# Kernel tuning notes

Hardware: AMD Instinct MI355X
Metric: run time of the kernel (lower is better)

The kernel has to match this reference:

```python
import jax, jax.numpy as jnp
import numpy as np

NUM_HEADS = 12


def get_rel_pos(q_size, k_size, rel_pos):
    # rel_pos: (2*max(q,k)-1, head_dim); sizes match table here so no resize.
    max_rel_dist = int(2 * max(q_size, k_size) - 1)
    if rel_pos.shape[0] != max_rel_dist:
        rel_pos = jax.image.resize(rel_pos, (max_rel_dist, rel_pos.shape[1]), method='linear')
    q_coords = jnp.arange(q_size)[:, None] * max(k_size / q_size, 1.0)
    k_coords = jnp.arange(k_size)[None, :] * max(q_size / k_size, 1.0)
    rel = (q_coords - k_coords + (k_size - 1) * max(q_size / k_size, 1.0)).astype(jnp.int32)
    return rel_pos[rel.reshape(-1)].reshape(q_size, k_size, -1)  # (q, k, head_dim)


def setup_inputs() -> dict:
    key = jax.random.key(0)
    ks = jax.random.split(key, 7)
    B, H, W, C = 8, 32, 32, 768
    head_dim = C // NUM_HEADS
    return {
        'x': jax.random.normal(ks[0], (B, H, W, C), jnp.float32),
        'w_qkv': jax.random.normal(ks[1], (C, 3 * C), jnp.float32) * 0.02,
        'b_qkv': jnp.zeros((3 * C,), jnp.float32),
        'rel_pos_h': jax.random.normal(ks[2], (2 * H - 1, head_dim), jnp.float32) * 0.02,
        'rel_pos_w': jax.random.normal(ks[3], (2 * W - 1, head_dim), jnp.float32) * 0.02,
        'w_proj': jax.random.normal(ks[4], (C, C), jnp.float32) * 0.02,
        'b_proj': jnp.zeros((C,), jnp.float32),
    }


def reference(x, w_qkv, b_qkv, rel_pos_h, rel_pos_w, w_proj, b_proj):
    B, H, W, C = x.shape
    heads = NUM_HEADS
    hd = C // heads
    S = H * W
    qkv = x @ w_qkv + b_qkv                                  # (B,H,W,3C)
    qkv = qkv.reshape(B, S, 3, heads, hd).transpose(2, 0, 3, 1, 4)
    qkv = qkv.reshape(3, B * heads, S, hd)
    q, k, v = qkv[0], qkv[1], qkv[2]
    attn = (q * hd ** -0.5) @ k.transpose(0, 2, 1)           # (B*heads, S, S)
    rh = get_rel_pos(H, H, rel_pos_h)                        # (H,H,hd)
    rw = get_rel_pos(W, W, rel_pos_w)                        # (W,W,hd)
    r_q = q.reshape(B * heads, H, W, hd)
    rel_h = jnp.einsum('bhwc,hkc->bhwk', r_q, rh)
    rel_w = jnp.einsum('bhwc,wkc->bhwk', r_q, rw)
    attn = (attn.reshape(B * heads, H, W, H, W)
            + rel_h[:, :, :, :, None]
            + rel_w[:, :, :, None, :]).reshape(B * heads, S, S)
    attn = jax.nn.softmax(attn, axis=-1)
    out = (attn @ v).reshape(B, heads, H, W, hd).transpose(0, 2, 3, 1, 4).reshape(B, H, W, C)
    return out @ w_proj + b_proj
```

## Files before the change

kernel.cpp:

```cpp
#include <hip/hip_runtime.h>
#include <hip/hip_bf16.h>

#define BATCH 8
#define SEQ   1024
#define CH    768
#define NH    12
#define HD    64
#define BH    96
#define N_QKV 2304

#define LOG2E 1.44269504088896f

typedef __attribute__((ext_vector_type(8))) short bfrag;
typedef __attribute__((ext_vector_type(4))) short short4v;
typedef __attribute__((ext_vector_type(4))) float ffrag;
typedef __attribute__((ext_vector_type(4))) int  intv4;

__device__ __forceinline__ short f2bf(float x) {
    __hip_bfloat16 h = __float2bfloat16(x);
    return *reinterpret_cast<short*>(&h);
}
__device__ __forceinline__ float bf2f(short b) {
    __hip_bfloat16 h;
    *reinterpret_cast<short*>(&h) = b;
    return __bfloat162float(h);
}
__device__ __forceinline__ void split2(float x, short& hi, short& lo) {
    short h = f2bf(x);
    hi = h;
    lo = f2bf(x - bf2f(h));
}
__device__ __forceinline__ void async_copy16(void* lds, const void* g) {
    __builtin_amdgcn_global_load_lds(
        (const __attribute__((address_space(1))) void*)g,
        (__attribute__((address_space(3))) void*)lds, 16, 0, 0);
}
__device__ __forceinline__ void pinned_load16(intv4& dst, const void* p) {
    asm volatile("global_load_dwordx4 %0, %1, off"
                 : "=&v"(dst) : "v"((unsigned long long)p));
}

__global__ __launch_bounds__(256) void prep(
    const float* __restrict__ x,
    const float* __restrict__ w_qkv, const float* __restrict__ w_proj,
    short* __restrict__ Xh,
    short* __restrict__ WqhT,
    short* __restrict__ WphT, short* __restrict__ WplT)
{
    __shared__ float ts[32][33];
    const int tid = threadIdx.x;
    const int bid = blockIdx.x;

    if (bid < 512) {
        const int n4 = (BATCH * SEQ * CH) / 4;
        for (int i = bid * 256 + tid; i < n4; i += 512 * 256) {
            float4 f = ((const float4*)x)[i];
            short4v h;
            h[0] = f2bf(f.x); h[1] = f2bf(f.y); h[2] = f2bf(f.z); h[3] = f2bf(f.w);
            ((short4v*)Xh)[i] = h;
        }
        return;
    }
    if (bid < 2240) {
        int t = bid - 512;
        const int bx = t % 72, by = t / 72;
        const int r0 = by * 32, c0 = bx * 32;
        #pragma unroll
        for (int i = 0; i < 4; ++i) {
            int idx = tid + i * 256;
            int rr = idx >> 5, cc = idx & 31;
            ts[rr][cc] = w_qkv[(size_t)(r0 + rr) * N_QKV + c0 + cc];
        }
        __syncthreads();
        #pragma unroll
        for (int i = 0; i < 4; ++i) {
            int idx = tid + i * 256;
            int rr = idx >> 5, cc = idx & 31;
            WqhT[(size_t)(c0 + rr) * CH + r0 + cc] = f2bf(ts[cc][rr]);
        }
        return;
    }
    {
        int t = bid - 2240;
        const int bx = t % 24, by = t / 24;
        const int r0 = by * 32, c0 = bx * 32;
        #pragma unroll
        for (int i = 0; i < 4; ++i) {
            int idx = tid + i * 256;
            int rr = idx >> 5, cc = idx & 31;
            ts[rr][cc] = w_proj[(size_t)(r0 + rr) * CH + c0 + cc];
        }
        __syncthreads();
        #pragma unroll
        for (int i = 0; i < 4; ++i) {
            int idx = tid + i * 256;
            int rr = idx >> 5, cc = idx & 31;
            short h, l;
            split2(ts[cc][rr], h, l);
            WphT[(size_t)(c0 + rr) * CH + r0 + cc] = h;
            WplT[(size_t)(c0 + rr) * CH + r0 + cc] = l;
        }
    }
}

__device__ __forceinline__ void gemm_core1(
    short* lds,
    const short* __restrict__ Ah, const short* __restrict__ BhT,
    int m0, int n0, ffrag acc[4][4])
{
    const int tid = threadIdx.x;
    const int wave = tid >> 6, lane = tid & 63;
    const int quad = lane >> 4, l16 = lane & 15;
    const int wm = (wave & 1) * 64, wn = (wave >> 1) * 64;

    const int arr  = wave >> 1;
    const int half = wave & 1;
    const short* src = arr ? BhT : Ah;
    const int row0 = (arr ? n0 : m0) + half * 64;
    const size_t lane_off = (size_t)(lane >> 3) * CH + (size_t)((lane & 7) ^ (lane >> 3)) * 8;
    const short* sbase = src + (size_t)row0 * CH + lane_off;
    short* ldsw = lds + arr * 8192 + half * 4096;

    for (int c = 0; c < 12; ++c) {
        __syncthreads();
        #pragma unroll
        for (int i = 0; i < 8; ++i)
            async_copy16(ldsw + i * 512, sbase + (size_t)i * 8 * CH + c * 64);
        __syncthreads();

        #pragma unroll
        for (int kc = 0; kc < 2; ++kc) {
            bfrag ah[4], bh[4];
            const int xs = ((kc * 4 + quad) ^ (l16 & 7)) * 8;
            #pragma unroll
            for (int i = 0; i < 4; ++i) {
                ah[i] = *(const bfrag*)&lds[(wm + i * 16 + l16) * 64 + xs];
                bh[i] = *(const bfrag*)&lds[8192 + (wn + i * 16 + l16) * 64 + xs];
            }
            #pragma unroll
            for (int mi = 0; mi < 4; ++mi)
                #pragma unroll
                for (int ni = 0; ni < 4; ++ni)
                    acc[mi][ni] = __builtin_amdgcn_mfma_f32_16x16x32_bf16(ah[mi], bh[ni], acc[mi][ni], 0, 0, 0);
        }
    }
}

__device__ __forceinline__ void gemm_core3(
    short* lds,
    const short* __restrict__ Ah, const short* __restrict__ Al,
    const short* __restrict__ BhT, const short* __restrict__ BlT,
    int m0, int n0, ffrag acc[4][4])
{
    const int tid = threadIdx.x;
    const int wave = tid >> 6, lane = tid & 63;
    const int quad = lane >> 4, l16 = lane & 15;
    const int wm = (wave & 1) * 64, wn = (wave >> 1) * 64;

    const short* src;
    int row0;
    if (wave == 0)      { src = Ah;  row0 = m0; }
    else if (wave == 1) { src = Al;  row0 = m0; }
    else if (wave == 2) { src = BhT; row0 = n0; }
    else                { src = BlT; row0 = n0; }
    const size_t lane_off = (size_t)(lane >> 3) * CH + (size_t)((lane & 7) ^ (lane >> 3)) * 8;
    const short* sbase = src + (size_t)row0 * CH + lane_off;
    short* ldsw = lds + wave * 8192;

    for (int c = 0; c < 12; ++c) {
        __syncthreads();
        #pragma unroll
        for (int i = 0; i < 16; ++i)
            async_copy16(ldsw + i * 512, sbase + (size_t)i * 8 * CH + c * 64);
        __syncthreads();

        #pragma unroll
        for (int kc = 0; kc < 2; ++kc) {
            bfrag ah[4], al[4], bh[4], bl[4];
            const int xs = ((kc * 4 + quad) ^ (l16 & 7)) * 8;
            #pragma unroll
            for (int i = 0; i < 4; ++i) {
                int ra = (wm + i * 16 + l16) * 64 + xs;
                int rb = (wn + i * 16 + l16) * 64 + xs;
                ah[i] = *(const bfrag*)&lds[ra];
                al[i] = *(const bfrag*)&lds[8192 + ra];
                bh[i] = *(const bfrag*)&lds[16384 + rb];
                bl[i] = *(const bfrag*)&lds[24576 + rb];
            }
            #pragma unroll
            for (int mi = 0; mi < 4; ++mi)
                #pragma unroll
                for (int ni = 0; ni < 4; ++ni) {
                    acc[mi][ni] = __builtin_amdgcn_mfma_f32_16x16x32_bf16(ah[mi], bh[ni], acc[mi][ni], 0, 0, 0);
                    acc[mi][ni] = __builtin_amdgcn_mfma_f32_16x16x32_bf16(ah[mi], bl[ni], acc[mi][ni], 0, 0, 0);
                    acc[mi][ni] = __builtin_amdgcn_mfma_f32_16x16x32_bf16(al[mi], bh[ni], acc[mi][ni], 0, 0, 0);
                }
        }
    }
}

__global__ __launch_bounds__(256) void gemm_qkv_mfma(
    const short* __restrict__ Xh,
    const short* __restrict__ WhT,
    const float* __restrict__ bias,
    short* __restrict__ qh, short* __restrict__ kh, short* __restrict__ vT)
{
    __shared__ short lds[2 * 8192];
    const int id  = blockIdx.x;
    const int xcd = id & 7;
    const int per = id >> 3;
    const int mi_ = per / 9, ni_ = per % 9;
    const int m0 = ((xcd & 3) * 16 + mi_) * 128;
    const int n0 = ((xcd >> 2) * 9 + ni_) * 128;
    const int which = n0 / CH;

    ffrag acc[4][4];
    #pragma unroll
    for (int i = 0; i < 4; ++i)
        #pragma unroll
        for (int j = 0; j < 4; ++j) acc[i][j] = (ffrag){0.f, 0.f, 0.f, 0.f};

    gemm_core1(lds, Xh, WhT, m0, n0, acc);

    const int tid = threadIdx.x;
    const int wave = tid >> 6, lane = tid & 63;
    const int quad = lane >> 4, l16 = lane & 15;
    const int wm = (wave & 1) * 64, wn = (wave >> 1) * 64;
    const int b = m0 >> 10;

    #pragma unroll
    for (int ni = 0; ni < 4; ++ni) {
        int n = n0 + wn + ni * 16 + l16;
        float bv = bias[n];
        int nin = n - which * CH;
        int head = nin >> 6, d = nin & 63;
        #pragma unroll
        for (int mi = 0; mi < 4; ++mi) {
            if (which == 2) {
                int s_base = (m0 & 1023) + wm + mi * 16 + quad * 4;
                short4v pk;
                #pragma unroll
                for (int r = 0; r < 4; ++r) pk[r] = f2bf(acc[mi][ni][r] + bv);
                *(short4v*)&vT[((size_t)(b * NH + head) * HD + d) * SEQ + s_base] = pk;
            } else {
                const float scale = (which == 0) ? 0.125f * LOG2E : 1.0f;
                short* dst = (which == 0) ? qh : kh;
                #pragma unroll
                for (int r = 0; r < 4; ++r) {
                    int m = m0 + wm + mi * 16 + quad * 4 + r;
                    int s = m & 1023;
                    dst[((size_t)(b * NH + head) * SEQ + s) * HD + d] =
                        f2bf((acc[mi][ni][r] + bv) * scale);
                }
            }
        }
    }
}

__global__ __launch_bounds__(256) void gemm_proj_mfma(
    const short* __restrict__ Ah, const short* __restrict__ Al,
    const short* __restrict__ WhT, const short* __restrict__ WlT,
    const float* __restrict__ bias, float* __restrict__ out)
{
    __shared__ short lds[4 * 8192];
    const int id  = blockIdx.x;
    const int xcd = id & 7;
    const int per = id >> 3;
    const int m0 = (xcd * 8 + per / 6) * 128;
    const int n0 = (per % 6) * 128;

    ffrag acc[4][4];
    #pragma unroll
    for (int i = 0; i < 4; ++i)
        #pragma unroll
        for (int j = 0; j < 4; ++j) acc[i][j] = (ffrag){0.f, 0.f, 0.f, 0.f};

    gemm_core3(lds, Ah, Al, WhT, WlT, m0, n0, acc);

    const int tid = threadIdx.x;
    const int wave = tid >> 6, lane = tid & 63;
    const int quad = lane >> 4, l16 = lane & 15;
    const int wm = (wave & 1) * 64, wn = (wave >> 1) * 64;

    #pragma unroll
    for (int ni = 0; ni < 4; ++ni) {
        int n = n0 + wn + ni * 16 + l16;
        float bv = bias[n];
        #pragma unroll
        for (int mi = 0; mi < 4; ++mi)
            #pragma unroll
            for (int r = 0; r < 4; ++r) {
                int m = m0 + wm + mi * 16 + quad * 4 + r;
                out[(size_t)m * CH + n] = acc[mi][ni][r] + bv;
            }
    }
}

__global__ __launch_bounds__(256, 3) void attn_kernel(
    const short* __restrict__ qh,
    const short* __restrict__ kh_g, const short* __restrict__ vT_g,
    const float* __restrict__ rph,
    const float* __restrict__ rpw,
    short* __restrict__ aoh, short* __restrict__ aol)
{
    const int fid   = blockIdx.x;
    const int xcd   = fid & 7;
    const int inner = fid >> 3;
    const int s0    = (inner & 7) * 128;
    const int bh    = xcd * 12 + (inner >> 3);

    const int tid  = threadIdx.x;
    const int wave = tid >> 6;
    const int lane = tid & 63;
    const int quad = lane >> 4;
    const int l16  = lane & 15;

    __shared__ short Kh[64 * 64];
    __shared__ short Vth[64 * 64];
    __shared__ short Th[128][68];
    __shared__ short Tw_Ps[128 * 68];

    const size_t bh_koff = (size_t)bh * SEQ * HD;
    const size_t bh_voff = (size_t)bh * HD * SEQ;
    const size_t klane = (size_t)(lane >> 3) * HD + (size_t)((lane & 7) ^ (lane >> 3)) * 8;
    const size_t vlane = (size_t)(lane >> 3) * SEQ + (size_t)((lane & 7) ^ (lane >> 3)) * 8;

    const short* kbase = kh_g + bh_koff + klane;
    const short* vbase = vT_g + bh_voff + vlane;
    const int i0 = wave * 2;
    short* KhW0 = Kh  + i0 * 512 + lane * 8;
    short* VtW0 = Vth + i0 * 512 + lane * 8;

    intv4 kA0, kA1, vA0, vA1, kB0, kB1, vB0, vB1;
    pinned_load16(kA0, kbase + (size_t)(i0 * 8) * HD);
    pinned_load16(kA1, kbase + (size_t)(i0 * 8 + 8) * HD);
    pinned_load16(vA0, vbase + (size_t)(i0 * 8) * SEQ);
    pinned_load16(vA1, vbase + (size_t)(i0 * 8 + 8) * SEQ);

    bfrag qfh[2][2];
    #pragma unroll
    for (int g = 0; g < 2; ++g) {
        const size_t qrow = ((size_t)bh * SEQ + s0 + wave * 32 + g * 16 + l16) * HD;
        #pragma unroll
        for (int kc = 0; kc < 2; ++kc)
            qfh[g][kc] = *(const bfrag*)(qh + qrow + kc * 32 + quad * 8);
    }

    #pragma unroll
    for (int table = 0; table < 2; ++table) {
        const float* tbl = table ? rpw : rph;
        #pragma unroll
        for (int n0r = 0; n0r < 64; n0r += 16) {
            int r = n0r + l16;
            bfrag bfr[2];
            #pragma unroll
            for (int kc = 0; kc < 2; ++kc) {
                if (r < 63) {
                    const float* trow = tbl + (size_t)r * HD + kc * 32 + quad * 8;
                    float4 f0 = *(const float4*)(trow);
                    float4 f1 = *(const float4*)(trow + 4);
                    float xs[8] = {f0.x, f0.y, f0.z, f0.w, f1.x, f1.y, f1.z, f1.w};
                    #pragma unroll
                    for (int j = 0; j < 8; ++j) bfr[kc][j] = f2bf(xs[j]);
                } else {
                    #pragma unroll
                    for (int j = 0; j < 8; ++j) bfr[kc][j] = 0;
                }
            }
            #pragma unroll
            for (int g = 0; g < 2; ++g) {
                ffrag acc = {0.f, 0.f, 0.f, 0.f};
                acc = __builtin_amdgcn_mfma_f32_16x16x32_bf16(qfh[g][0], bfr[0], acc, 0, 0, 0);
                acc = __builtin_amdgcn_mfma_f32_16x16x32_bf16(qfh[g][1], bfr[1], acc, 0, 0, 0);
                int row = wave * 32 + g * 16 + quad * 4;
                #pragma unroll
                for (int reg = 0; reg < 4; ++reg) {
                    short v = f2bf(acc[reg] * 8.0f);
                    if (table) Tw_Ps[(row + reg) * 68 + n0r + l16] = v;
                    else       Th[row + reg][n0r + l16] = v;
                }
            }
        }
    }

    float tw_r[2][2][4];
    #pragma unroll
    for (int g = 0; g < 2; ++g) {
        int qloc = wave * 32 + g * 16 + l16;
        int wq = g * 16 + l16;
        #pragma unroll
        for (int p = 0; p < 2; ++p)
            #pragma unroll
            for (int reg = 0; reg < 4; ++reg)
                tw_r[g][p][reg] = bf2f(Tw_Ps[qloc * 68 + (wq - (p * 16 + quad * 4 + reg) + 31)]);
    }
    const int hq_w = (s0 >> 5) + wave;

    float l_part[2] = {0.f, 0.f};
    ffrag Ot[2][4];
    #pragma unroll
    for (int g = 0; g < 2; ++g)
        #pragma unroll
        for (int t = 0; t < 4; ++t) Ot[g][t] = (ffrag){0.f, 0.f, 0.f, 0.f};

    auto chunk = [&](int c, const intv4& ck0, const intv4& ck1,
                     const intv4& cv0, const intv4& cv1,
                     intv4& nk0, intv4& nk1, intv4& nv0, intv4& nv1) {
        __syncthreads();
        if (c < 15) {
            const int cn = c + 1;
            pinned_load16(nk0, kbase + (size_t)(cn * 64 + i0 * 8) * HD);
            pinned_load16(nk1, kbase + (size_t)(cn * 64 + i0 * 8 + 8) * HD);
            pinned_load16(nv0, vbase + (size_t)(i0 * 8) * SEQ + cn * 64);
            pinned_load16(nv1, vbase + (size_t)(i0 * 8 + 8) * SEQ + cn * 64);
            asm volatile("s_waitcnt vmcnt(4)");
        } else {
            asm volatile("s_waitcnt vmcnt(0)");
        }
        __builtin_amdgcn_sched_barrier(0);
        *(intv4*)KhW0         = ck0;
        *(intv4*)(KhW0 + 512) = ck1;
        *(intv4*)VtW0         = cv0;
        *(intv4*)(VtW0 + 512) = cv1;
        __syncthreads();

        float th_r[2][2];
        #pragma unroll
        for (int g = 0; g < 2; ++g) {
            int qloc = wave * 32 + g * 16 + l16;
            th_r[g][0] = bf2f(Th[qloc][hq_w - 2 * c + 31]);
            th_r[g][1] = bf2f(Th[qloc][hq_w - 2 * c - 1 + 31]);
        }

        #pragma unroll
        for (int kt = 0; kt < 4; ++kt) {
            bfrag kbh[2];
            #pragma unroll
            for (int kc = 0; kc < 2; ++kc) {
                int xs = ((kc * 4 + quad) ^ (l16 & 7)) * 8;
                kbh[kc] = *(const bfrag*)&Kh[(kt * 16 + l16) * 64 + xs];
            }
            const int hp = kt >> 1, wp = kt & 1;
            #pragma unroll
            for (int g = 0; g < 2; ++g) {
                ffrag acc;
                #pragma unroll
                for (int reg = 0; reg < 4; ++reg)
                    acc[reg] = th_r[g][hp] + tw_r[g][wp][reg];
                __builtin_amdgcn_s_setprio(1);
                acc = __builtin_amdgcn_mfma_f32_16x16x32_bf16(kbh[0], qfh[g][0], acc, 0, 0, 0);
                acc = __builtin_amdgcn_mfma_f32_16x16x32_bf16(kbh[1], qfh[g][1], acc, 0, 0, 0);
                __builtin_amdgcn_s_setprio(0);
                short4v pk;
                #pragma unroll
                for (int reg = 0; reg < 4; ++reg) {
                    float p = exp2f(acc[reg]);
                    l_part[g] += p;
                    pk[reg] = f2bf(p);
                }
                *(short4v*)&Tw_Ps[(wave * 32 + g * 16 + l16) * 68 + kt * 16 + quad * 4] = pk;
            }
        }

        bfrag pf[2][2];
        #pragma unroll
        for (int g = 0; g < 2; ++g)
            #pragma unroll
            for (int kc2 = 0; kc2 < 2; ++kc2) {
                int base = (wave * 32 + g * 16 + l16) * 68 + kc2 * 32 + quad * 8;
                short4v lo = *(const short4v*)&Tw_Ps[base];
                short4v hi = *(const short4v*)&Tw_Ps[base + 4];
                bfrag p;
                #pragma unroll
                for (int j = 0; j < 4; ++j) { p[j] = lo[j]; p[j + 4] = hi[j]; }
                pf[g][kc2] = p;
            }

        #pragma unroll
        for (int t = 0; t < 4; ++t) {
            int d = t * 16 + l16;
            int x0 = ((0 + quad) ^ (l16 & 7)) * 8;
            int x1 = ((4 + quad) ^ (l16 & 7)) * 8;
            bfrag vh0 = *(const bfrag*)&Vth[d * 64 + x0];
            bfrag vh1 = *(const bfrag*)&Vth[d * 64 + x1];
            __builtin_amdgcn_s_setprio(1);
            #pragma unroll
            for (int g = 0; g < 2; ++g) {
                Ot[g][t] = __builtin_amdgcn_mfma_f32_16x16x32_bf16(pf[g][0], vh0, Ot[g][t], 0, 0, 0);
                Ot[g][t] = __builtin_amdgcn_mfma_f32_16x16x32_bf16(pf[g][1], vh1, Ot[g][t], 0, 0, 0);
            }
            __builtin_amdgcn_s_setprio(0);
        }
    };

    for (int cc = 0; cc < 8; ++cc) {
        chunk(2 * cc,     kA0, kA1, vA0, vA1, kB0, kB1, vB0, vB1);
        chunk(2 * cc + 1, kB0, kB1, vB0, vB1, kA0, kA1, vA0, vA1);
    }

    {
        int b = bh / NH, head = bh % NH;
        #pragma unroll
        for (int g = 0; g < 2; ++g) {
            float r = l_part[g];
            r += __shfl_xor(r, 16, 64);
            r += __shfl_xor(r, 32, 64);
            float invl = 1.f / r;
            float inv[4];
            #pragma unroll
            for (int reg = 0; reg < 4; ++reg)
                inv[reg] = __shfl(invl, quad * 4 + reg, 16);
            #pragma unroll
            for (int t = 0; t < 4; ++t) {
                #pragma unroll
                for (int reg = 0; reg < 4; ++reg) {
                    int s_ = s0 + wave * 32 + g * 16 + quad * 4 + reg;
                    int d = t * 16 + l16;
                    size_t idx = ((size_t)(b * SEQ + s_)) * CH + head * HD + d;
                    short h, l;
                    split2(Ot[g][t][reg] * inv[reg], h, l);
                    aoh[idx] = h;
                    aol[idx] = l;
                }
            }
        }
    }
}

extern "C" void kernel_launch(void* const* d_in, const int* in_sizes, int n_in,
                              void* d_out, int out_size, void* d_ws, size_t ws_size,
                              hipStream_t stream) {
    const float* x       = (const float*)d_in[0];
    const float* w_qkv   = (const float*)d_in[1];
    const float* b_qkv   = (const float*)d_in[2];
    const float* rph     = (const float*)d_in[3];
    const float* rpw     = (const float*)d_in[4];
    const float* w_proj  = (const float*)d_in[5];
    const float* b_proj  = (const float*)d_in[6];
    float* out = (float*)d_out;

    const size_t NTOK = (size_t)BATCH * SEQ;
    const size_t XSZ  = NTOK * CH;
    const size_t WQSZ = (size_t)N_QKV * CH;
    const size_t WPSZ = (size_t)CH * CH;
    short* Xh   = (short*)d_ws;
    short* AoL  = Xh + XSZ;
    short* WqhT = AoL + XSZ;
    short* WphT = WqhT + WQSZ;
    short* WplT = WphT + WPSZ;
    short* qh = WplT + WPSZ;
    short* kh = qh + XSZ;
    short* vT = kh + XSZ;
    short* aoh = Xh;
    short* aol = AoL;

    prep<<<dim3(2816), 256, 0, stream>>>(x, w_qkv, w_proj,
                                         Xh, WqhT, WphT, WplT);
    gemm_qkv_mfma<<<dim3(1152), 256, 0, stream>>>(Xh, WqhT, b_qkv,
                                                  qh, kh, vT);
    attn_kernel<<<dim3(768), 256, 0, stream>>>(qh, kh, vT,
                                               rph, rpw, aoh, aol);
    gemm_proj_mfma<<<dim3(384), 256, 0, stream>>>(aoh, aol, WphT, WplT,
                                                  b_proj, out);
}
```

Measured before the change: 223.4 us.

## Feed softmax probabilities to PV MFMA from registers via permuted V layout

Stops writing the exponentiated probability tile to LDS and reading it back as an A-operand. Pairs of score tiles are now computed together, and their outputs are packed directly into the bf16 fragment for the P*V MFMA. V is written to LDS in a permuted, swizzled order (split 8-byte stores) so its K-index ordering matches the register layout of P. This removes an LDS round-trip per chunk and shortens the dependency chain, at the cost of more, smaller LDS stores for V and more live registers.

```diff
diff --git a/kernel.cpp b/kernel.cpp
--- a/kernel.cpp
+++ b/kernel.cpp
@@ -15,6 +15,7 @@
 typedef __attribute__((ext_vector_type(4))) short short4v;
 typedef __attribute__((ext_vector_type(4))) float ffrag;
 typedef __attribute__((ext_vector_type(4))) int  intv4;
+typedef __attribute__((ext_vector_type(2))) int  intv2;
 
 __device__ __forceinline__ short f2bf(float x) {
     __hip_bfloat16 h = __float2bfloat16(x);
@@ -323,19 +324,32 @@
     const size_t bh_koff = (size_t)bh * SEQ * HD;
     const size_t bh_voff = (size_t)bh * HD * SEQ;
     const size_t klane = (size_t)(lane >> 3) * HD + (size_t)((lane & 7) ^ (lane >> 3)) * 8;
-    const size_t vlane = (size_t)(lane >> 3) * SEQ + (size_t)((lane & 7) ^ (lane >> 3)) * 8;
 
     const short* kbase = kh_g + bh_koff + klane;
-    const short* vbase = vT_g + bh_voff + vlane;
     const int i0 = wave * 2;
-    short* KhW0 = Kh  + i0 * 512 + lane * 8;
-    short* VtW0 = Vth + i0 * 512 + lane * 8;
+    short* KhW0 = Kh + i0 * 512 + lane * 8;
+
+    const short* vgbase = vT_g + bh_voff
+        + (size_t)(wave * 16 + (lane >> 3)) * SEQ + (size_t)(lane & 7) * 8;
+
+    int vwA[2], vwB[2];
+    {
+        const int m  = lane & 7;
+        const int oA = ((m >> 2) << 2) + ((m & 1) << 1);
+        const int hf = (m >> 1) & 1;
+        #pragma unroll
+        for (int jj = 0; jj < 2; ++jj) {
+            int d = wave * 16 + jj * 8 + (lane >> 3);
+            vwA[jj] = d * 64 + ((oA ^ (d & 7)) << 3) + hf * 4;
+            vwB[jj] = d * 64 + (((oA + 1) ^ (d & 7)) << 3) + hf * 4;
+        }
+    }
 
     intv4 kA0, kA1, vA0, vA1, kB0, kB1, vB0, vB1;
     pinned_load16(kA0, kbase + (size_t)(i0 * 8) * HD);
     pinned_load16(kA1, kbase + (size_t)(i0 * 8 + 8) * HD);
-    pinned_load16(vA0, vbase + (size_t)(i0 * 8) * SEQ);
-    pinned_load16(vA1, vbase + (size_t)(i0 * 8 + 8) * SEQ);
+    pinned_load16(vA0, vgbase);
+    pinned_load16(vA1, vgbase + (size_t)8 * SEQ);
 
     bfrag qfh[2][2];
     #pragma unroll
@@ -411,8 +425,8 @@
             const int cn = c + 1;
             pinned_load16(nk0, kbase + (size_t)(cn * 64 + i0 * 8) * HD);
             pinned_load16(nk1, kbase + (size_t)(cn * 64 + i0 * 8 + 8) * HD);
-            pinned_load16(nv0, vbase + (size_t)(i0 * 8) * SEQ + cn * 64);
-            pinned_load16(nv1, vbase + (size_t)(i0 * 8 + 8) * SEQ + cn * 64);
+            pinned_load16(nv0, vgbase + cn * 64);
+            pinned_load16(nv1, vgbase + (size_t)8 * SEQ + cn * 64);
             asm volatile("s_waitcnt vmcnt(4)");
         } else {
             asm volatile("s_waitcnt vmcnt(0)");
@@ -420,8 +434,14 @@
         __builtin_amdgcn_sched_barrier(0);
         *(intv4*)KhW0         = ck0;
         *(intv4*)(KhW0 + 512) = ck1;
-        *(intv4*)VtW0         = cv0;
-        *(intv4*)(VtW0 + 512) = cv1;
+        {
+            intv2 lo0 = {cv0[0], cv0[1]}, hi0 = {cv0[2], cv0[3]};
+            intv2 lo1 = {cv1[0], cv1[1]}, hi1 = {cv1[2], cv1[3]};
+            *(intv2*)&Vth[vwA[0]] = lo0;
+            *(intv2*)&Vth[vwB[0]] = hi0;
+            *(intv2*)&Vth[vwA[1]] = lo1;
+            *(intv2*)&Vth[vwB[1]] = hi1;
+        }
         __syncthreads();
 
         float th_r[2][2];
@@ -433,63 +453,49 @@
         }
 
         #pragma unroll
-        for (int kt = 0; kt < 4; ++kt) {
-            bfrag kbh[2];
+        for (int ktp = 0; ktp < 2; ++ktp) {
+            bfrag kbhE[2], kbhO[2];
             #pragma unroll
             for (int kc = 0; kc < 2; ++kc) {
                 int xs = ((kc * 4 + quad) ^ (l16 & 7)) * 8;
-                kbh[kc] = *(const bfrag*)&Kh[(kt * 16 + l16) * 64 + xs];
-            }
-            const int hp = kt >> 1, wp = kt & 1;
+                kbhE[kc] = *(const bfrag*)&Kh[((2 * ktp) * 16 + l16) * 64 + xs];
+                kbhO[kc] = *(const bfrag*)&Kh[((2 * ktp + 1) * 16 + l16) * 64 + xs];
+            }
+            bfrag pf[2];
             #pragma unroll
             for (int g = 0; g < 2; ++g) {
-                ffrag acc;
-                #pragma unroll
-                for (int reg = 0; reg < 4; ++reg)
-                    acc[reg] = th_r[g][hp] + tw_r[g][wp][reg];
+                ffrag aE, aO;
+                #pragma unroll
+                for (int reg = 0; reg < 4; ++reg) {
+                    aE[reg] = th_r[g][ktp] + tw_r[g][0][reg];
+                    aO[reg] = th_r[g][ktp] + tw_r[g][1][reg];
+                }
                 __builtin_amdgcn_s_setprio(1);
-                acc = __builtin_amdgcn_mfma_f32_16x16x32_bf16(kbh[0], qfh[g][0], acc, 0, 0, 0);
-                acc = __builtin_amdgcn_mfma_f32_16x16x32_bf16(kbh[1], qfh[g][1], acc, 0, 0, 0);
+                aE = __builtin_amdgcn_mfma_f32_16x16x32_bf16(kbhE[0], qfh[g][0], aE, 0, 0, 0);
+                aE = __builtin_amdgcn_mfma_f32_16x16x32_bf16(kbhE[1], qfh[g][1], aE, 0, 0, 0);
+                aO = __builtin_amdgcn_mfma_f32_16x16x32_bf16(kbhO[0], qfh[g][0], aO, 0, 0, 0);
+                aO = __builtin_amdgcn_mfma_f32_16x16x32_bf16(kbhO[1], qfh[g][1], aO, 0, 0, 0);
                 __builtin_amdgcn_s_setprio(0);
-                short4v pk;
                 #pragma unroll
                 for (int reg = 0; reg < 4; ++reg) {
-                    float p = exp2f(acc[reg]);
-                    l_part[g] += p;
-                    pk[reg] = f2bf(p);
-                }
-                *(short4v*)&Tw_Ps[(wave * 32 + g * 16 + l16) * 68 + kt * 16 + quad * 4] = pk;
-            }
-        }
-
-        bfrag pf[2][2];
-        #pragma unroll
-        for (int g = 0; g < 2; ++g)
-            #pragma unroll
-            for (int kc2 = 0; kc2 < 2; ++kc2) {
-                int base = (wave * 32 + g * 16 + l16) * 68 + kc2 * 32 + quad * 8;
-                short4v lo = *(const short4v*)&Tw_Ps[base];
-                short4v hi = *(const short4v*)&Tw_Ps[base + 4];
-                bfrag p;
-                #pragma unroll
-                for (int j = 0; j < 4; ++j) { p[j] = lo[j]; p[j + 4] = hi[j]; }
-                pf[g][kc2] = p;
-            }
-
-        #pragma unroll
-        for (int t = 0; t < 4; ++t) {
-            int d = t * 16 + l16;
-            int x0 = ((0 + quad) ^ (l16 & 7)) * 8;
-            int x1 = ((4 + quad) ^ (l16 & 7)) * 8;
-            bfrag vh0 = *(const bfrag*)&Vth[d * 64 + x0];
-            bfrag vh1 = *(const bfrag*)&Vth[d * 64 + x1];
-            __builtin_amdgcn_s_setprio(1);
-            #pragma unroll
-            for (int g = 0; g < 2; ++g) {
-                Ot[g][t] = __builtin_amdgcn_mfma_f32_16x16x32_bf16(pf[g][0], vh0, Ot[g][t], 0, 0, 0);
-                Ot[g][t] = __builtin_amdgcn_mfma_f32_16x16x32_bf16(pf[g][1], vh1, Ot[g][t], 0, 0, 0);
-            }
-            __builtin_amdgcn_s_setprio(0);
+                    float pE = exp2f(aE[reg]);
+                    float pO = exp2f(aO[reg]);
+                    l_part[g] += pE + pO;
+                    pf[g][reg]     = f2bf(pE);
+                    pf[g][reg + 4] = f2bf(pO);
+                }
+            }
+            #pragma unroll
+            for (int t = 0; t < 4; ++t) {
+                int d = t * 16 + l16;
+                int xv = ((ktp * 4 + quad) ^ (l16 & 7)) * 8;
+                bfrag vh = *(const bfrag*)&Vth[d * 64 + xv];
+                __builtin_amdgcn_s_setprio(1);
+                #pragma unroll
+                for (int g = 0; g < 2; ++g)
+                    Ot[g][t] = __builtin_amdgcn_mfma_f32_16x16x32_bf16(pf[g], vh, Ot[g][t], 0, 0, 0);
+                __builtin_amdgcn_s_setprio(0);
+            }
         }
     };
 
```

After: 224.4 us. No clear change (+0.5%).
